# Performance work log

Hardware: AMD Instinct MI355X
Metric: run time of the kernel (lower is better)

## Reference

```python
import jax, jax.numpy as jnp
import numpy as np

D_MODEL = 1024
HIDDEN = 2048            # hidden_dimension // num_smaller_experts_per_expert
E_ROUTED = 14            # total_num_experts*num_smaller - num_shared
E_SHARED = 2
TOP_K = 2                # num_activated*num_smaller - num_shared
EPS = 1e-9               # config.epsilon
RMS_EPS = 1.1920929e-07  # torch RMSNorm default eps=None -> finfo(float32).eps


def setup_inputs() -> dict:
    key = jax.random.key(0)
    ks = jax.random.split(key, 9)
    B, T = 2, 1024
    x = jax.random.normal(ks[0], (B, T, D_MODEL), dtype=jnp.float32)
    router_w = jax.random.normal(ks[1], (D_MODEL, E_ROUTED), dtype=jnp.float32) * 0.006
    rms_w = jnp.ones((E_ROUTED, D_MODEL), dtype=jnp.float32)
    w1 = jax.random.normal(ks[2], (E_ROUTED, D_MODEL, HIDDEN), dtype=jnp.float32) * 0.02
    w2 = jax.random.normal(ks[3], (E_ROUTED, HIDDEN, D_MODEL), dtype=jnp.float32) * 0.02
    rms_w_s = jnp.ones((E_SHARED, D_MODEL), dtype=jnp.float32)
    w1_s = jax.random.normal(ks[4], (E_SHARED, D_MODEL, HIDDEN), dtype=jnp.float32) * 0.02
    w2_s = jax.random.normal(ks[5], (E_SHARED, HIDDEN, D_MODEL), dtype=jnp.float32) * 0.02
    return {"x": x, "router_w": router_w, "rms_w": rms_w, "w1": w1, "w2": w2,
            "rms_w_s": rms_w_s, "w1_s": w1_s, "w2_s": w2_s}


def _ffn(xn, rw, W1, W2):
    # RMSNorm -> Linear -> SiLU -> Linear (dropout is identity in eval)
    ms = jnp.mean(xn * xn, axis=-1, keepdims=True)
    h = (xn * jax.lax.rsqrt(ms + RMS_EPS)) * rw
    return jax.nn.silu(h @ W1) @ W2


def reference(x, router_w, rms_w, w1, w2, rms_w_s, w1_s, w2_s):
    B, T, D = x.shape
    N = B * T
    xf = x.reshape(N, D)
    # router gates + top-k sparsification + renormalization
    gates = jax.nn.softmax(xf @ router_w, axis=-1)          # [N, E]
    top_v, top_i = jax.lax.top_k(gates, TOP_K)              # [N, K]
    masked = jnp.zeros_like(gates).at[jnp.arange(N)[:, None], top_i].set(top_v)
    masked = masked / (masked.sum(axis=-1, keepdims=True) + EPS)  # [N, E]
    # routed experts: compute each expert on all tokens, combine with sparse gate weights
    # (same math as dispatch/index_add combine since masked is 0 off the top-k)
    routed = jax.vmap(lambda rw_, W1_, W2_: _ffn(xf, rw_, W1_, W2_))(rms_w, w1, w2)  # [E, N, D]
    routed_out = jnp.einsum('end,ne->nd', routed, masked)
    # shared experts: unweighted sum
    shared = jax.vmap(lambda rw_, W1_, W2_: _ffn(xf, rw_, W1_, W2_))(rms_w_s, w1_s, w2_s).sum(0)
    return (routed_out + shared).reshape(B, T, D)
```

## Files before the change

kernel.cpp:

```cpp
#include <hip/hip_runtime.h>
#include <hip/hip_bf16.h>
#include <cstdint>
#include <cstddef>

#define D_MODEL 1024
#define HIDDEN 2048
#define E_ROUTED 14
#define E_TOT 16
#define NTOK 2048
#define NASSIGN 4096
#define NROWS 8192
#define GEMM_NWG 768

typedef __bf16 bf16x8 __attribute__((ext_vector_type(8)));
typedef float f32x4 __attribute__((ext_vector_type(4)));

static __device__ __forceinline__ unsigned short f2b(float f) {
  unsigned int u = __builtin_bit_cast(unsigned int, f);
  u += 0x7fffu + ((u >> 16) & 1u);
  return (unsigned short)(u >> 16);
}

#define ASYNC_COPY16(gptr, lptr)                                                        \
  __builtin_amdgcn_global_load_lds(                                                     \
      (const __attribute__((address_space(1))) unsigned int*)(gptr),                    \
      (__attribute__((address_space(3))) unsigned int*)(lptr), 16, 0, 0)

__global__ __launch_bounds__(256) void router_kernel(
    const float* __restrict__ x, const float* __restrict__ rweight,
    int* __restrict__ topi, float* __restrict__ topw,
    unsigned short* __restrict__ xhat) {
  int n = blockIdx.x, tid = threadIdx.x;
  const float4 xv = reinterpret_cast<const float4*>(x + (size_t)n * D_MODEL)[tid];
  float ss = xv.x * xv.x + xv.y * xv.y + xv.z * xv.z + xv.w * xv.w;
  float lg[E_ROUTED];
#pragma unroll
  for (int e = 0; e < E_ROUTED; ++e) lg[e] = 0.f;
  const float xa[4] = {xv.x, xv.y, xv.z, xv.w};
#pragma unroll
  for (int i = 0; i < 4; ++i) {
    const float* rw = rweight + (size_t)(tid * 4 + i) * E_ROUTED;
    float xd = xa[i];
#pragma unroll
    for (int e = 0; e < E_ROUTED; ++e) lg[e] = fmaf(xd, rw[e], lg[e]);
  }
#pragma unroll
  for (int off = 32; off > 0; off >>= 1) {
    ss += __shfl_xor(ss, off);
#pragma unroll
    for (int e = 0; e < E_ROUTED; ++e) lg[e] += __shfl_xor(lg[e], off);
  }
  __shared__ float red[4][16];
  int wid = tid >> 6, lane = tid & 63;
  if (lane == 0) {
    red[wid][0] = ss;
#pragma unroll
    for (int e = 0; e < E_ROUTED; ++e) red[wid][1 + e] = lg[e];
  }
  __syncthreads();
  __shared__ float s_scale;
  if (tid == 0) {
    float fin[15];
    for (int v = 0; v < 15; ++v) fin[v] = red[0][v] + red[1][v] + red[2][v] + red[3][v];
    s_scale = rsqrtf(fin[0] * (1.f / D_MODEL) + 1.1920929e-07f);
    float mx = fin[1];
    for (int e = 1; e < E_ROUTED; ++e) mx = fmaxf(mx, fin[1 + e]);
    float p[E_ROUTED]; float Z = 0.f;
    for (int e = 0; e < E_ROUTED; ++e) { p[e] = __expf(fin[1 + e] - mx); Z += p[e]; }
    int i0 = 0; float v0 = p[0];
    for (int e = 1; e < E_ROUTED; ++e) if (p[e] > v0) { v0 = p[e]; i0 = e; }
    int i1 = (i0 == 0) ? 1 : 0; float v1 = p[i1];
    for (int e = 0; e < E_ROUTED; ++e) if (e != i0 && p[e] > v1) { v1 = p[e]; i1 = e; }
    v0 /= Z; v1 /= Z;
    float inv = 1.f / (v0 + v1 + 1e-9f);
    topi[2 * n] = i0; topi[2 * n + 1] = i1;
    topw[2 * n] = v0 * inv; topw[2 * n + 1] = v1 * inv;
  }
  __syncthreads();
  float sc = s_scale;
  ushort4 hx;
  hx.x = f2b(xv.x * sc); hx.y = f2b(xv.y * sc);
  hx.z = f2b(xv.z * sc); hx.w = f2b(xv.w * sc);
  reinterpret_cast<ushort4*>(xhat + (size_t)n * D_MODEL)[tid] = hx;
}

__global__ __launch_bounds__(256) void count_kernel(const int* __restrict__ topi,
                                                    int* __restrict__ goff,
                                                    int* __restrict__ cursor,
                                                    int* __restrict__ base1,
                                                    int* __restrict__ base2) {
  __shared__ int cnt[E_ROUTED];
  int tid = threadIdx.x;
  if (tid < E_ROUTED) cnt[tid] = 0;
  __syncthreads();
  for (int i = tid; i < NASSIGN; i += 256) atomicAdd(&cnt[topi[i]], 1);
  __syncthreads();
  if (tid == 0) {
    int acc = 0;
    for (int e = 0; e < E_ROUTED; ++e) { goff[e] = acc; cursor[e] = acc; acc += cnt[e]; }
    goff[E_ROUTED] = acc;
    int b1 = 0, b2 = 0;
    for (int g = 0; g < E_TOT; ++g) {
      base1[g] = b1; base2[g] = b2;
      int c = (g < E_ROUTED) ? cnt[g] : NTOK;
      int mt = (c + 127) >> 7;
      b1 += mt * (HIDDEN / 128);
      b2 += mt * (D_MODEL / 128);
    }
    base1[E_TOT] = b1; base2[E_TOT] = b2;
  }
}

__global__ __launch_bounds__(256) void scatter_kernel(
    const int* __restrict__ topi, const float* __restrict__ topw,
    int* __restrict__ cursor, int* __restrict__ row_token,
    float* __restrict__ row_gate, int* __restrict__ token_rows) {
  int i = blockIdx.x * 256 + threadIdx.x;
  if (i >= NASSIGN) return;
  int e = topi[i];
  int pos = atomicAdd(&cursor[e], 1);
  row_token[pos] = i >> 1;
  row_gate[pos] = topw[i];
  token_rows[i] = pos;
}

template <int K, int N, bool SCALE>
__global__ __launch_bounds__(256) void convT_kernel(
    const float* __restrict__ Wr, const float* __restrict__ Ws,
    const float* __restrict__ RWr, const float* __restrict__ RWs,
    unsigned short* __restrict__ outT) {
  __shared__ float tile[64][65];
  int g = blockIdx.z;
  const float* src = (g < E_ROUTED) ? Wr + (size_t)g * K * N
                                    : Ws + (size_t)(g - E_ROUTED) * K * N;
  const float* rw = nullptr;
  if constexpr (SCALE)
    rw = (g < E_ROUTED) ? RWr + (size_t)g * K : RWs + (size_t)(g - E_ROUTED) * K;
  int k0 = blockIdx.y * 64, nn0 = blockIdx.x * 64;
  int t = threadIdx.x;
  int kk = t >> 4, nc = (t & 15) * 4;
#pragma unroll
  for (int j = 0; j < 4; ++j) {
    int k = kk + j * 16;
    float4 v = *(const float4*)(src + (size_t)(k0 + k) * N + nn0 + nc);
    float s = 1.f;
    if constexpr (SCALE) s = rw[k0 + k];
    tile[k][nc]     = v.x * s;
    tile[k][nc + 1] = v.y * s;
    tile[k][nc + 2] = v.z * s;
    tile[k][nc + 3] = v.w * s;
  }
  __syncthreads();
  int k8 = (t & 7) * 8;
#pragma unroll
  for (int p = 0; p < 2; ++p) {
    int n = (t >> 3) + p * 32;
    uint4 pk;
    pk.x = (unsigned)f2b(tile[k8 + 0][n]) | ((unsigned)f2b(tile[k8 + 1][n]) << 16);
    pk.y = (unsigned)f2b(tile[k8 + 2][n]) | ((unsigned)f2b(tile[k8 + 3][n]) << 16);
    pk.z = (unsigned)f2b(tile[k8 + 4][n]) | ((unsigned)f2b(tile[k8 + 5][n]) << 16);
    pk.w = (unsigned)f2b(tile[k8 + 6][n]) | ((unsigned)f2b(tile[k8 + 7][n]) << 16);
    *(uint4*)(outT + ((size_t)g * N + nn0 + n) * K + k0 + k8) = pk;
  }
}

template <bool G1, int KTOT, int NTOT>
__global__ __launch_bounds__(256, 3) void ffn_gemm(
    const int* __restrict__ goff, const int* __restrict__ base,
    const int* __restrict__ row_token, const float* __restrict__ row_gate,
    const unsigned short* __restrict__ Abase,
    const unsigned short* __restrict__ Wt,
    unsigned short* __restrict__ Hout, float* __restrict__ Yout) {
  __shared__ __align__(16) char smem[32 * 1024];
  __shared__ int sbase[E_TOT + 1];
  __shared__ int sgoff[E_ROUTED + 1];

  int tid = threadIdx.x, lane = tid & 63, wid = tid >> 6;
  if (tid <= E_TOT) sbase[tid] = base[tid];
  if (tid >= 32 && tid <= 32 + E_ROUTED) sgoff[tid - 32] = goff[tid - 32];
  __syncthreads();

  int xcd = blockIdx.x & 7, slot = blockIdx.x >> 3;
  int total = sbase[E_TOT];
  int chunk = (total + 7) >> 3;
  int cend = min((xcd + 1) * chunk, total);

  int wr = (wid >> 1) * 64, wc = (wid & 1) * 64;
  int lrow = lane >> 3;
  int swz = lrow << 4;
  int colB = ((lane & 7) << 4) ^ swz;
  int l15 = lane & 15;

  for (int c = xcd * chunk + slot; c < cend; c += (GEMM_NWG >> 3)) {
    int g = 0;
    while (sbase[g + 1] <= c) ++g;
    int grpStart, cnt;
    if (g < E_ROUTED) { grpStart = sgoff[g]; cnt = sgoff[g + 1] - sgoff[g]; }
    else { grpStart = NASSIGN + (g - E_ROUTED) * NTOK; cnt = NTOK; }
    int mtg = (cnt + 127) >> 7;
    int r = c - sbase[g];
    int nxb = r / mtg;
    int myb = r - nxb * mtg;
    int m0 = myb * 128, n0 = nxb * 128;

    char* sA = smem;
    char* sB = smem + 16 * 1024;
    const char* aSrc[4];
    const char* bSrc[4];
#pragma unroll
    for (int i = 0; i < 4; ++i) {
      int row = wid * 32 + i * 8 + lrow;
      int rIdx = m0 + row; if (rIdx >= cnt) rIdx = cnt - 1;
      int srcRow;
      if constexpr (G1) srcRow = (g < E_ROUTED) ? row_token[grpStart + rIdx] : rIdx;
      else srcRow = grpStart + rIdx;
      aSrc[i] = (const char*)(Abase + (size_t)srcRow * KTOT) + colB;
      bSrc[i] = (const char*)(Wt + ((size_t)g * NTOT + n0 + row) * KTOT) + colB;
    }

    f32x4 acc[4][4];
#pragma unroll
    for (int m = 0; m < 4; ++m)
#pragma unroll
      for (int n = 0; n < 4; ++n)
#pragma unroll
        for (int cc = 0; cc < 4; ++cc) acc[m][n][cc] = 0.f;

    for (int kt = 0; kt < KTOT / 64; ++kt) {
#pragma unroll
      for (int i = 0; i < 4; ++i) ASYNC_COPY16(aSrc[i], sA + wid * 4096 + i * 1024);
#pragma unroll
      for (int i = 0; i < 4; ++i) ASYNC_COPY16(bSrc[i], sB + wid * 4096 + i * 1024);
#pragma unroll
      for (int i = 0; i < 4; ++i) { aSrc[i] += 128; bSrc[i] += 128; }
      __syncthreads();

#pragma unroll
      for (int ks = 0; ks < 2; ++ks) {
        int kb = ks * 64 + ((lane >> 4) << 4);
        bf16x8 af[4], bfr[4];
#pragma unroll
        for (int m = 0; m < 4; ++m) {
          int rr = wr + m * 16 + l15;
          af[m] = *(const bf16x8*)(sA + (rr << 7) + (kb ^ ((rr & 7) << 4)));
        }
#pragma unroll
        for (int n = 0; n < 4; ++n) {
          int rr = wc + n * 16 + l15;
          bfr[n] = *(const bf16x8*)(sB + (rr << 7) + (kb ^ ((rr & 7) << 4)));
        }
#pragma unroll
        for (int m = 0; m < 4; ++m)
#pragma unroll
          for (int n = 0; n < 4; ++n)
            acc[m][n] = __builtin_amdgcn_mfma_f32_16x16x32_bf16(af[m], bfr[n], acc[m][n], 0, 0, 0);
      }
      __syncthreads();
    }

    int lr = (lane >> 4) * 4;
#pragma unroll
    for (int m = 0; m < 4; ++m) {
      int rloc = m0 + wr + m * 16 + lr;
#pragma unroll
      for (int j = 0; j < 4; ++j) {
        if (rloc + j < cnt) {
          size_t rg = (size_t)(grpStart + rloc + j);
          if constexpr (G1) {
#pragma unroll
            for (int n = 0; n < 4; ++n) {
              float v = acc[m][n][j];
              float sv = v / (1.f + __expf(-v));
              Hout[rg * HIDDEN + (n0 + wc + n * 16 + l15)] = f2b(sv);
            }
          } else {
            float gate = 1.f;
            if (g < E_ROUTED) gate = row_gate[rg];
#pragma unroll
            for (int n = 0; n < 4; ++n)
              Yout[rg * D_MODEL + (n0 + wc + n * 16 + l15)] = acc[m][n][j] * gate;
          }
        }
      }
    }
  }
}

__global__ __launch_bounds__(256) void combine_kernel(
    const float* __restrict__ y, const int* __restrict__ token_rows,
    float* __restrict__ out) {
  int n = blockIdx.x, tid = threadIdx.x;
  int a0 = token_rows[2 * n], a1 = token_rows[2 * n + 1];
  const float4* y0 = reinterpret_cast<const float4*>(y + (size_t)a0 * D_MODEL);
  const float4* y1 = reinterpret_cast<const float4*>(y + (size_t)a1 * D_MODEL);
  const float4* s0 = reinterpret_cast<const float4*>(y + (size_t)(NASSIGN + n) * D_MODEL);
  const float4* s1 = reinterpret_cast<const float4*>(y + (size_t)(NASSIGN + NTOK + n) * D_MODEL);
  float4 a = y0[tid], b = y1[tid], c = s0[tid], d = s1[tid];
  float4 r;
  r.x = a.x + b.x + c.x + d.x;
  r.y = a.y + b.y + c.y + d.y;
  r.z = a.z + b.z + c.z + d.z;
  r.w = a.w + b.w + c.w + d.w;
  reinterpret_cast<float4*>(out + (size_t)n * D_MODEL)[tid] = r;
}

extern "C" void kernel_launch(void* const* d_in, const int* in_sizes, int n_in,
                              void* d_out, int out_size, void* d_ws, size_t ws_size,
                              hipStream_t stream) {
  const float* x        = (const float*)d_in[0];
  const float* router_w = (const float*)d_in[1];
  const float* rms_w    = (const float*)d_in[2];
  const float* w1       = (const float*)d_in[3];
  const float* w2       = (const float*)d_in[4];
  const float* rms_w_s  = (const float*)d_in[5];
  const float* w1_s    = (const float*)d_in[6];
  const float* w2_s    = (const float*)d_in[7];
  float* out = (float*)d_out;

  char* ws = (char*)d_ws;
  unsigned short* xhat = (unsigned short*)ws;
  unsigned short* h    = (unsigned short*)(ws + ((size_t)4 << 20));
  float* y             = (float*)(ws + ((size_t)36 << 20));
  unsigned short* w1t  = (unsigned short*)(ws + ((size_t)68 << 20));
  unsigned short* w2t  = (unsigned short*)(ws + ((size_t)132 << 20));
  char* meta = ws + ((size_t)196 << 20);
  int*   topi       = (int*)(meta);
  float* topw       = (float*)(meta + (16 << 10));
  int*   row_token  = (int*)(meta + (32 << 10));
  float* row_gate   = (float*)(meta + (48 << 10));
  int*   token_rows = (int*)(meta + (64 << 10));
  int*   goff       = (int*)(meta + (80 << 10));
  int*   cursor     = (int*)(meta + (80 << 10) + 128);
  int*   base1      = (int*)(meta + (80 << 10) + 256);
  int*   base2      = (int*)(meta + (80 << 10) + 384);

  router_kernel<<<NTOK, 256, 0, stream>>>(x, router_w, topi, topw, xhat);
  count_kernel<<<1, 256, 0, stream>>>(topi, goff, cursor, base1, base2);
  scatter_kernel<<<NASSIGN / 256, 256, 0, stream>>>(topi, topw, cursor, row_token,
                                                    row_gate, token_rows);
  convT_kernel<D_MODEL, HIDDEN, true><<<dim3(HIDDEN / 64, D_MODEL / 64, E_TOT), 256, 0, stream>>>(
      w1, w1_s, rms_w, rms_w_s, w1t);
  convT_kernel<HIDDEN, D_MODEL, false><<<dim3(D_MODEL / 64, HIDDEN / 64, E_TOT), 256, 0, stream>>>(
      w2, w2_s, nullptr, nullptr, w2t);
  ffn_gemm<true, D_MODEL, HIDDEN><<<GEMM_NWG, 256, 0, stream>>>(
      goff, base1, row_token, row_gate, xhat, w1t, h, nullptr);
  ffn_gemm<false, HIDDEN, D_MODEL><<<GEMM_NWG, 256, 0, stream>>>(
      goff, base2, row_token, row_gate, h, w2t, nullptr, y);
  combine_kernel<<<NTOK, 256, 0, stream>>>(y, token_rows, out);
}
```

Baseline: 232.8 us.

## Widen GEMM tiles to 128x256 and split-K the second FFN GEMM

Each workgroup now computes a 128x256 output tile, with every wave owning a 64-column slice and all 128 rows. This raises MFMA work per A-tile load. The down-projection GEMM is split along K into two halves written to separate y buffers, and the combine kernel sums both partials. The aim is better operand reuse and enough tiles to keep workgroups busy in the second GEMM, at the cost of more accumulator registers, more LDS, and extra fp32 partial-output traffic.

```diff
diff --git a/kernel.cpp b/kernel.cpp
--- a/kernel.cpp
+++ b/kernel.cpp
@@ -104,8 +104,8 @@
       base1[g] = b1; base2[g] = b2;
       int c = (g < E_ROUTED) ? cnt[g] : NTOK;
       int mt = (c + 127) >> 7;
-      b1 += mt * (HIDDEN / 128);
-      b2 += mt * (D_MODEL / 128);
+      b1 += mt * (HIDDEN / 256);
+      b2 += mt * (D_MODEL / 256) * 2;
     }
     base1[E_TOT] = b1; base2[E_TOT] = b2;
   }
@@ -164,14 +164,16 @@
   }
 }
 
-template <bool G1, int KTOT, int NTOT>
+template <bool G1, int KROW, int NTOT, int KSL>
 __global__ __launch_bounds__(256, 3) void ffn_gemm(
     const int* __restrict__ goff, const int* __restrict__ base,
     const int* __restrict__ row_token, const float* __restrict__ row_gate,
     const unsigned short* __restrict__ Abase,
     const unsigned short* __restrict__ Wt,
     unsigned short* __restrict__ Hout, float* __restrict__ Yout) {
-  __shared__ __align__(16) char smem[32 * 1024];
+  constexpr int NT = 16;
+
+  __shared__ __align__(16) char smem[48 * 1024];
   __shared__ int sbase[E_TOT + 1];
   __shared__ int sgoff[E_ROUTED + 1];
 
@@ -185,10 +187,8 @@
   int chunk = (total + 7) >> 3;
   int cend = min((xcd + 1) * chunk, total);
 
-  int wr = (wid >> 1) * 64, wc = (wid & 1) * 64;
   int lrow = lane >> 3;
-  int swz = lrow << 4;
-  int colB = ((lane & 7) << 4) ^ swz;
+  int colB = ((lane & 7) << 4) ^ (lrow << 4);
   int l15 = lane & 15;
 
   for (int c = xcd * chunk + slot; c < cend; c += (GEMM_NWG >> 3)) {
@@ -199,14 +199,15 @@
     else { grpStart = NASSIGN + (g - E_ROUTED) * NTOK; cnt = NTOK; }
     int mtg = (cnt + 127) >> 7;
     int r = c - sbase[g];
-    int nxb = r / mtg;
-    int myb = r - nxb * mtg;
-    int m0 = myb * 128, n0 = nxb * 128;
+    int nxb, myb, ksl = 0;
+    if constexpr (KSL > 1) { ksl = r / (4 * mtg); int r2 = r - ksl * 4 * mtg; nxb = r2 / mtg; myb = r2 - nxb * mtg; }
+    else { nxb = r / mtg; myb = r - nxb * mtg; }
+    int m0 = myb * 128, n0 = nxb * 256, kOff = ksl * 1024;
 
     char* sA = smem;
     char* sB = smem + 16 * 1024;
     const char* aSrc[4];
-    const char* bSrc[4];
+    const char* bSrc[8];
 #pragma unroll
     for (int i = 0; i < 4; ++i) {
       int row = wid * 32 + i * 8 + lrow;
@@ -214,71 +215,76 @@
       int srcRow;
       if constexpr (G1) srcRow = (g < E_ROUTED) ? row_token[grpStart + rIdx] : rIdx;
       else srcRow = grpStart + rIdx;
-      aSrc[i] = (const char*)(Abase + (size_t)srcRow * KTOT) + colB;
-      bSrc[i] = (const char*)(Wt + ((size_t)g * NTOT + n0 + row) * KTOT) + colB;
-    }
-
-    f32x4 acc[4][4];
-#pragma unroll
-    for (int m = 0; m < 4; ++m)
+      aSrc[i] = (const char*)(Abase + (size_t)srcRow * KROW + kOff) + colB;
+    }
+#pragma unroll
+    for (int i = 0; i < 8; ++i) {
+      int row = wid * 64 + i * 8 + lrow;
+      bSrc[i] = (const char*)(Wt + ((size_t)g * NTOT + n0 + row) * KROW + kOff) + colB;
+    }
+
+    f32x4 acc[8][4];
+#pragma unroll
+    for (int m = 0; m < 8; ++m)
 #pragma unroll
       for (int n = 0; n < 4; ++n)
 #pragma unroll
         for (int cc = 0; cc < 4; ++cc) acc[m][n][cc] = 0.f;
 
-    for (int kt = 0; kt < KTOT / 64; ++kt) {
+    for (int kt = 0; kt < NT; ++kt) {
 #pragma unroll
       for (int i = 0; i < 4; ++i) ASYNC_COPY16(aSrc[i], sA + wid * 4096 + i * 1024);
 #pragma unroll
-      for (int i = 0; i < 4; ++i) ASYNC_COPY16(bSrc[i], sB + wid * 4096 + i * 1024);
-#pragma unroll
-      for (int i = 0; i < 4; ++i) { aSrc[i] += 128; bSrc[i] += 128; }
+      for (int i = 0; i < 8; ++i) ASYNC_COPY16(bSrc[i], sB + wid * 8192 + i * 1024);
+#pragma unroll
+      for (int i = 0; i < 4; ++i) aSrc[i] += 128;
+#pragma unroll
+      for (int i = 0; i < 8; ++i) bSrc[i] += 128;
       __syncthreads();
 
 #pragma unroll
       for (int ks = 0; ks < 2; ++ks) {
         int kb = ks * 64 + ((lane >> 4) << 4);
-        bf16x8 af[4], bfr[4];
-#pragma unroll
-        for (int m = 0; m < 4; ++m) {
-          int rr = wr + m * 16 + l15;
-          af[m] = *(const bf16x8*)(sA + (rr << 7) + (kb ^ ((rr & 7) << 4)));
+        bf16x8 bfr[4];
+#pragma unroll
+        for (int nf = 0; nf < 4; ++nf) {
+          int rr = wid * 64 + nf * 16 + l15;
+          bfr[nf] = *(const bf16x8*)(sB + (rr << 7) + (kb ^ ((rr & 7) << 4)));
         }
 #pragma unroll
-        for (int n = 0; n < 4; ++n) {
-          int rr = wc + n * 16 + l15;
-          bfr[n] = *(const bf16x8*)(sB + (rr << 7) + (kb ^ ((rr & 7) << 4)));
+        for (int mf = 0; mf < 8; ++mf) {
+          int rr = mf * 16 + l15;
+          bf16x8 a = *(const bf16x8*)(sA + (rr << 7) + (kb ^ ((rr & 7) << 4)));
+#pragma unroll
+          for (int nf = 0; nf < 4; ++nf)
+            acc[mf][nf] = __builtin_amdgcn_mfma_f32_16x16x32_bf16(a, bfr[nf], acc[mf][nf], 0, 0, 0);
         }
-#pragma unroll
-        for (int m = 0; m < 4; ++m)
-#pragma unroll
-          for (int n = 0; n < 4; ++n)
-            acc[m][n] = __builtin_amdgcn_mfma_f32_16x16x32_bf16(af[m], bfr[n], acc[m][n], 0, 0, 0);
       }
       __syncthreads();
     }
 
     int lr = (lane >> 4) * 4;
 #pragma unroll
-    for (int m = 0; m < 4; ++m) {
-      int rloc = m0 + wr + m * 16 + lr;
+    for (int mf = 0; mf < 8; ++mf) {
+      int rloc = m0 + mf * 16 + lr;
 #pragma unroll
       for (int j = 0; j < 4; ++j) {
         if (rloc + j < cnt) {
           size_t rg = (size_t)(grpStart + rloc + j);
           if constexpr (G1) {
 #pragma unroll
-            for (int n = 0; n < 4; ++n) {
-              float v = acc[m][n][j];
+            for (int nf = 0; nf < 4; ++nf) {
+              float v = acc[mf][nf][j];
               float sv = v / (1.f + __expf(-v));
-              Hout[rg * HIDDEN + (n0 + wc + n * 16 + l15)] = f2b(sv);
+              Hout[rg * HIDDEN + (n0 + wid * 64 + nf * 16 + l15)] = f2b(sv);
             }
           } else {
             float gate = 1.f;
             if (g < E_ROUTED) gate = row_gate[rg];
-#pragma unroll
-            for (int n = 0; n < 4; ++n)
-              Yout[rg * D_MODEL + (n0 + wc + n * 16 + l15)] = acc[m][n][j] * gate;
+            float* yo = Yout + (size_t)ksl * NROWS * D_MODEL;
+#pragma unroll
+            for (int nf = 0; nf < 4; ++nf)
+              yo[rg * D_MODEL + (n0 + wid * 64 + nf * 16 + l15)] = acc[mf][nf][j] * gate;
           }
         }
       }
@@ -291,16 +297,19 @@
     float* __restrict__ out) {
   int n = blockIdx.x, tid = threadIdx.x;
   int a0 = token_rows[2 * n], a1 = token_rows[2 * n + 1];
-  const float4* y0 = reinterpret_cast<const float4*>(y + (size_t)a0 * D_MODEL);
-  const float4* y1 = reinterpret_cast<const float4*>(y + (size_t)a1 * D_MODEL);
-  const float4* s0 = reinterpret_cast<const float4*>(y + (size_t)(NASSIGN + n) * D_MODEL);
-  const float4* s1 = reinterpret_cast<const float4*>(y + (size_t)(NASSIGN + NTOK + n) * D_MODEL);
-  float4 a = y0[tid], b = y1[tid], c = s0[tid], d = s1[tid];
-  float4 r;
-  r.x = a.x + b.x + c.x + d.x;
-  r.y = a.y + b.y + c.y + d.y;
-  r.z = a.z + b.z + c.z + d.z;
-  r.w = a.w + b.w + c.w + d.w;
+  float4 r = {0.f, 0.f, 0.f, 0.f};
+#pragma unroll
+  for (int ks = 0; ks < 2; ++ks) {
+    const float* yb = y + (size_t)ks * NROWS * D_MODEL;
+    float4 a = reinterpret_cast<const float4*>(yb + (size_t)a0 * D_MODEL)[tid];
+    float4 b = reinterpret_cast<const float4*>(yb + (size_t)a1 * D_MODEL)[tid];
+    float4 c = reinterpret_cast<const float4*>(yb + (size_t)(NASSIGN + n) * D_MODEL)[tid];
+    float4 d = reinterpret_cast<const float4*>(yb + (size_t)(NASSIGN + NTOK + n) * D_MODEL)[tid];
+    r.x += a.x + b.x + c.x + d.x;
+    r.y += a.y + b.y + c.y + d.y;
+    r.z += a.z + b.z + c.z + d.z;
+    r.w += a.w + b.w + c.w + d.w;
+  }
   reinterpret_cast<float4*>(out + (size_t)n * D_MODEL)[tid] = r;
 }
 
@@ -342,9 +351,9 @@
       w1, w1_s, rms_w, rms_w_s, w1t);
   convT_kernel<HIDDEN, D_MODEL, false><<<dim3(D_MODEL / 64, HIDDEN / 64, E_TOT), 256, 0, stream>>>(
       w2, w2_s, nullptr, nullptr, w2t);
-  ffn_gemm<true, D_MODEL, HIDDEN><<<GEMM_NWG, 256, 0, stream>>>(
+  ffn_gemm<true, D_MODEL, HIDDEN, 1><<<GEMM_NWG, 256, 0, stream>>>(
       goff, base1, row_token, row_gate, xhat, w1t, h, nullptr);
-  ffn_gemm<false, HIDDEN, D_MODEL><<<GEMM_NWG, 256, 0, stream>>>(
+  ffn_gemm<false, HIDDEN, D_MODEL, 2><<<GEMM_NWG, 256, 0, stream>>>(
       goff, base2, row_token, row_gate, h, w2t, nullptr, y);
   combine_kernel<<<NTOK, 256, 0, stream>>>(y, token_rows, out);
 }
```

After: 330.4 us. 1.42x slower.
